# Kernel tuning notes

Measured on AMD Instinct MI355X. Metric: run time of the kernel, lower is better.

The kernel has to match this reference:

```python
import jax, jax.numpy as jnp
import numpy as np

B, T, DH, EH = 512, 64, 512, 512  # batch, window, decoder_hidden, encoder_hidden


def setup_inputs() -> dict:
    key = jax.random.key(0)
    ks = jax.random.split(key, 16)
    s = lambda *sh: 1.0 / np.sqrt(sh[-1])
    inp = {
        "X_encoded": jax.random.normal(ks[0], (B, T - 1, EH), dtype=jnp.float32),
        "y_prev": jax.random.normal(ks[1], (B, T - 1), dtype=jnp.float32),
        # attn_layer: Linear(2*DH+EH -> EH), Tanh, Linear(EH -> 1)
        "attn_W1": jax.random.normal(ks[2], (EH, 2 * DH + EH), dtype=jnp.float32) * s(2 * DH + EH),
        "attn_b1": jnp.zeros((EH,), jnp.float32),
        "attn_W2": jax.random.normal(ks[3], (1, EH), dtype=jnp.float32) * s(EH),
        "attn_b2": jnp.zeros((1,), jnp.float32),
        # fc: Linear(EH+1 -> 1), weights init normal_() in original
        "fc_W": jax.random.normal(ks[4], (1, EH + 1), dtype=jnp.float32),
        "fc_b": jnp.zeros((1,), jnp.float32),
        # LSTM(input_size=1, hidden=DH): gate order i,f,g,o
        "W_ih": jax.random.normal(ks[5], (4 * DH, 1), dtype=jnp.float32) * s(DH),
        "W_hh": jax.random.normal(ks[6], (4 * DH, DH), dtype=jnp.float32) * s(DH),
        "b_ih": jnp.zeros((4 * DH,), jnp.float32),
        "b_hh": jnp.zeros((4 * DH,), jnp.float32),
        # final heads: Linear(DH+EH -> 1) x3
        "beta_W": jax.random.normal(ks[7], (1, DH + EH), dtype=jnp.float32) * s(DH + EH),
        "beta_b": jnp.zeros((1,), jnp.float32),
        "gamma_W": jax.random.normal(ks[8], (1, DH + EH), dtype=jnp.float32) * s(DH + EH),
        "gamma_b": jnp.zeros((1,), jnp.float32),
        "sigma_W": jax.random.normal(ks[9], (1, DH + EH), dtype=jnp.float32) * s(DH + EH),
        "sigma_b": jnp.zeros((1,), jnp.float32),
    }
    return inp


def reference(X_encoded, y_prev, attn_W1, attn_b1, attn_W2, attn_b2, fc_W, fc_b,
              W_ih, W_hh, b_ih, b_hh, beta_W, beta_b, gamma_W, gamma_b, sigma_W, sigma_b):
    Bn, Tm1, eh = X_encoded.shape
    dh = W_hh.shape[1]

    def step(carry, y_t):
        d, c = carry  # [B, DH] each
        dc = jnp.concatenate([d, c], axis=-1)                      # [B, 2DH]
        x = jnp.concatenate(
            [jnp.broadcast_to(dc[:, None, :], (Bn, Tm1, 2 * dh)), X_encoded], axis=-1
        )                                                           # [B, T-1, 2DH+EH]
        h = jnp.tanh(jnp.einsum('bte,fe->btf', x, attn_W1) + attn_b1)
        scores = (jnp.einsum('btf,of->bto', h, attn_W2) + attn_b2)[..., 0]  # [B, T-1]
        beta = jax.nn.softmax(scores, axis=1)
        ctx = jnp.einsum('bt,bte->be', beta, X_encoded)             # [B, EH]
        y_tilde = jnp.concatenate([ctx, y_t[:, None]], axis=1) @ fc_W.T + fc_b  # [B, 1]
        gates = y_tilde @ W_ih.T + b_ih + d @ W_hh.T + b_hh        # [B, 4DH]
        i, f, g, o = jnp.split(gates, 4, axis=-1)
        c_new = jax.nn.sigmoid(f) * c + jax.nn.sigmoid(i) * jnp.tanh(g)
        d_new = jax.nn.sigmoid(o) * jnp.tanh(c_new)
        return (d_new, c_new), ctx

    init = (jnp.zeros((Bn, dh), X_encoded.dtype), jnp.zeros((Bn, dh), X_encoded.dtype))
    (d, c), ctxs = jax.lax.scan(step, init, y_prev.T)  # scan over T-1 steps
    ctx_last = ctxs[-1]                                # context from final iteration (pre-update d,c)
    final = jnp.concatenate([d, ctx_last], axis=1)     # [B, DH+EH]
    y_beta = final @ beta_W.T + beta_b
    y_gamma = final @ gamma_W.T + gamma_b
    y_sigma = final @ sigma_W.T + sigma_b
    return (y_beta, y_sigma, y_gamma)
```

## Files before the change

kernel.cpp:

```cpp
#include <hip/hip_runtime.h>

typedef __bf16 bf16x8 __attribute__((ext_vector_type(8)));
typedef float  f32x4  __attribute__((ext_vector_type(4)));

#define Bn  512
#define TM1 63

__device__ __forceinline__ float fast_rcp(float x){ return __builtin_amdgcn_rcpf(x); }
__device__ __forceinline__ float fast_tanh(float x){
    float e = __expf(2.0f*x);
    return 1.0f - 2.0f*fast_rcp(e + 1.0f);
}
__device__ __forceinline__ float fast_sigmoid(float x){
    return fast_rcp(1.0f + __expf(-x));
}

__device__ __forceinline__ void gll16(const __bf16* g, __bf16* l) {
    __builtin_amdgcn_global_load_lds(
        (const __attribute__((address_space(1))) unsigned int*)(g),
        (__attribute__((address_space(3))) unsigned int*)(l),
        16, 0, 0);
}


__global__ __launch_bounds__(256) void k_prep_weights(
    const float* __restrict__ W1, const float* __restrict__ Whh_f,
    const float* __restrict__ b_ih, const float* __restrict__ b_hh,
    __bf16* __restrict__ Wdc, __bf16* __restrict__ W1x, __bf16* __restrict__ Whh,
    float* __restrict__ bsum)
{
    int i = blockIdx.x*256 + threadIdx.x;
    int n = gridDim.x*256;
    for (int idx = i; idx < 512*1024; idx += n) {
        int f = idx >> 10, k = idx & 1023;
        Wdc[idx] = (__bf16)W1[f*1536 + k];
    }
    for (int idx = i; idx < 512*512; idx += n) {
        int f = idx >> 9, k = idx & 511;
        W1x[idx] = (__bf16)W1[f*1536 + 1024 + k];
    }
    for (int idx = i; idx < 2048*512; idx += n) {
        Whh[idx] = (__bf16)Whh_f[idx];
    }
    for (int idx = i; idx < 2048; idx += n) {
        bsum[idx] = b_ih[idx] + b_hh[idx];
    }
}

__global__ __launch_bounds__(256) void k_conv_x(const float* __restrict__ X, __bf16* __restrict__ Xb, int n)
{
    int idx = (blockIdx.x*256 + threadIdx.x)*4;
    if (idx < n) {
        float4 v = *(const float4*)(X + idx);
        Xb[idx+0] = (__bf16)v.x; Xb[idx+1] = (__bf16)v.y;
        Xb[idx+2] = (__bf16)v.z; Xb[idx+3] = (__bf16)v.w;
    }
}

__global__ __launch_bounds__(256) void k_xf(
    const __bf16* __restrict__ Xbf, const float* __restrict__ fcW, float* __restrict__ XF)
{
    int lane = threadIdx.x & 63, wave = threadIdx.x >> 6;
    float fcr[8];
    {
        const float4* fp = (const float4*)(fcW + lane*8);
        float4 f0 = fp[0], f1 = fp[1];
        fcr[0]=f0.x; fcr[1]=f0.y; fcr[2]=f0.z; fcr[3]=f0.w;
        fcr[4]=f1.x; fcr[5]=f1.y; fcr[6]=f1.z; fcr[7]=f1.w;
    }
    int row0 = (blockIdx.x*4 + wave)*8;
    #pragma unroll
    for (int j = 0; j < 8; ++j) {
        int row = row0 + j;
        if (row >= Bn*TM1) break;
        bf16x8 x = *(const bf16x8*)(Xbf + (size_t)row*512 + lane*8);
        float p = 0.f;
        #pragma unroll
        for (int i=0;i<8;i++) p += fcr[i]*(float)x[i];
        #pragma unroll
        for (int o=32;o;o>>=1) p += __shfl_xor(p,o,64);
        if (lane==0) XF[row] = p;
    }
}

template <int ADDBIAS>
__device__ __forceinline__ void gemm_tile_lds(
    const __bf16* __restrict__ A, const __bf16* __restrict__ Bm,
    const float* __restrict__ bias, void* __restrict__ C, int as_bf16,
    int row0, int col0, int K, int lda, int ldb, int ldc,
    __bf16* sA, __bf16* sB)
{
    int lane = threadIdx.x & 63, wave = threadIdx.x >> 6;
    int wr = wave >> 1, wc = wave & 1;
    int l15 = lane & 15, l4 = lane >> 4;
    int lr = lane >> 3;
    int lcs = ((lane & 7) ^ lr) * 8;

    auto stage = [&](int buf, int kt) {
        int k0 = kt*64;
        #pragma unroll
        for (int j = 0; j < 2; ++j) {
            int c = wave*2 + j;
            int grow = c*8 + lr;
            gll16(A  + (size_t)(row0+grow)*lda + k0 + lcs, sA + buf*4096 + c*512);
            gll16(Bm + (size_t)(col0+grow)*ldb + k0 + lcs, sB + buf*4096 + c*512);
        }
    };

    int NT = K >> 6;
    stage(0, 0);
    f32x4 acc[2][2] = {};
    int s7 = l15 & 7;
    const __bf16* aRow = sA + (wr*32 + l15)*64;
    const __bf16* bRow = sB + (wc*32 + l15)*64;
    for (int kt = 0; kt < NT; ++kt) {
        int buf = kt & 1;
        asm volatile("s_waitcnt vmcnt(0)");
        __syncthreads();
        if (kt + 1 < NT) stage(buf ^ 1, kt + 1);
        #pragma unroll
        for (int kk = 0; kk < 2; ++kk) {
            int ch = ((l4 + kk*4) ^ s7) * 8;
            bf16x8 a0 = *(const bf16x8*)(aRow + buf*4096 + ch);
            bf16x8 a1 = *(const bf16x8*)(aRow + buf*4096 + 16*64 + ch);
            bf16x8 b0 = *(const bf16x8*)(bRow + buf*4096 + ch);
            bf16x8 b1 = *(const bf16x8*)(bRow + buf*4096 + 16*64 + ch);
            acc[0][0] = __builtin_amdgcn_mfma_f32_16x16x32_bf16(a0,b0,acc[0][0],0,0,0);
            acc[0][1] = __builtin_amdgcn_mfma_f32_16x16x32_bf16(a0,b1,acc[0][1],0,0,0);
            acc[1][0] = __builtin_amdgcn_mfma_f32_16x16x32_bf16(a1,b0,acc[1][0],0,0,0);
            acc[1][1] = __builtin_amdgcn_mfma_f32_16x16x32_bf16(a1,b1,acc[1][1],0,0,0);
        }
    }
    int row_a = row0 + wr*32;
    int col_b = col0 + wc*32;
    #pragma unroll
    for (int mi=0; mi<2; mi++)
    #pragma unroll
    for (int ni=0; ni<2; ni++) {
        int r0 = row_a + mi*16 + l4*4;
        int c0 = col_b + ni*16 + l15;
        float bv = ADDBIAS ? bias[c0] : 0.f;
        if (as_bf16) {
            __bf16* Cb = (__bf16*)C;
            #pragma unroll
            for (int r=0; r<4; r++)
                Cb[(size_t)(r0+r)*ldc + c0] = (__bf16)(acc[mi][ni][r] + bv);
        } else {
            float* Cf = (float*)C;
            #pragma unroll
            for (int r=0; r<4; r++)
                Cf[(size_t)(r0+r)*ldc + c0] = acc[mi][ni][r];
        }
    }
}

__global__ __launch_bounds__(256) void k_gemm_xw(
    const __bf16* __restrict__ A, const __bf16* __restrict__ Bm,
    const float* __restrict__ bias, __bf16* __restrict__ C)
{
    __shared__ __bf16 sA[2*4096], sB[2*4096];
    int orig = (blockIdx.x & 7)*504 + (blockIdx.x >> 3);
    int tm = orig >> 3, tn = orig & 7;
    gemm_tile_lds<1>(A, Bm, bias, C, 1, tm*64, tn*64, 512, 512, 512, 512, sA, sB);
}

__global__ __launch_bounds__(256) void k_step_gemm(
    const __bf16* __restrict__ dc, const __bf16* __restrict__ Wdc,
    const __bf16* __restrict__ Whh, __bf16* __restrict__ dcWp, __bf16* __restrict__ dWhhp)
{
    __shared__ __bf16 sA[2*4096], sB[2*4096];
    int blk = blockIdx.x;
    if (blk < 256) {
        int kh = blk & 3, tt = blk >> 2;
        int tm = tt >> 3, tn = tt & 7;
        gemm_tile_lds<0>(dc + kh*256, Wdc + kh*256, nullptr,
                         dcWp + (size_t)kh*512*512, 1,
                         tm*64, tn*64, 256, 1024, 1024, 512, sA, sB);
    } else {
        int b2 = blk - 256;
        int kh = b2 & 1, tt = b2 >> 1;
        int tm = tt >> 5, tn = tt & 31;
        gemm_tile_lds<0>(dc + kh*256, Whh + kh*256, nullptr,
                         dWhhp + (size_t)kh*512*2048, 1,
                         tm*64, tn*64, 256, 1024, 512, 2048, sA, sB);
    }
}


#define PSTR 76
__global__ __launch_bounds__(512) void k_step_fused(
    int t,
    const __bf16* __restrict__ dcWp, const __bf16* __restrict__ dWhhp,
    const __bf16* __restrict__ XWb, const float* __restrict__ XF,
    const float* __restrict__ y_prev, const float* __restrict__ W2,
    const float* __restrict__ fcW, const float* __restrict__ fcb,
    const float* __restrict__ W_ih, const float* __restrict__ bsum,
    float* __restrict__ c_f32, float* __restrict__ d_f32,
    __bf16* __restrict__ dc_bf16, float* __restrict__ beta_out)
{
    int b = blockIdx.x;
    int tid = threadIdx.x, lane = tid & 63, wave = tid >> 6;
    __shared__ float s_part[64*PSTR];
    __shared__ float s_sc[64];
    __shared__ float s_y;

    size_t gb = (size_t)b*2048 + tid;
    const __bf16* dW0 = dWhhp;
    const __bf16* dW1 = dWhhp + (size_t)512*2048;
    float pg_i = (float)dW0[gb]        + (float)dW1[gb];
    float pg_f = (float)dW0[gb + 512]  + (float)dW1[gb + 512];
    float pg_g = (float)dW0[gb + 1024] + (float)dW1[gb + 1024];
    float pg_o = (float)dW0[gb + 1536] + (float)dW1[gb + 1536];
    float wi_i = W_ih[tid];
    float wi_f = W_ih[512 + tid];
    float wi_g = W_ih[1024 + tid];
    float wi_o = W_ih[1536 + tid];
    float bs_i = bsum[tid];
    float bs_f = bsum[512 + tid];
    float bs_g = bsum[1024 + tid];
    float bs_o = bsum[1536 + tid];
    float c_old = c_f32[(size_t)b*512 + tid];

    float w2r[8], dr[8];
    {
        const float4* w2p = (const float4*)(W2 + lane*8);
        float4 w0 = w2p[0], w1 = w2p[1];
        w2r[0]=w0.x; w2r[1]=w0.y; w2r[2]=w0.z; w2r[3]=w0.w;
        w2r[4]=w1.x; w2r[5]=w1.y; w2r[6]=w1.z; w2r[7]=w1.w;
        #pragma unroll
        for (int i=0;i<8;i++) dr[i] = 0.f;
        #pragma unroll
        for (int q=0;q<4;q++) {
            bf16x8 a = *(const bf16x8*)(dcWp + (size_t)q*512*512 + (size_t)b*512 + lane*8);
            #pragma unroll
            for (int i=0;i<8;i++) dr[i] += (float)a[i];
        }
    }
    {
        const __bf16* xwp = XWb + ((size_t)b*TM1 + wave*8)*512 + lane*8;
        #pragma unroll
        for (int j = 0; j < 8; ++j) {
            int tt = wave*8 + j;
            float p = 0.f;
            if (tt < TM1) {
                bf16x8 xw = *(const bf16x8*)(xwp + (size_t)j*512);
                #pragma unroll
                for (int i=0;i<8;i++) p += w2r[i]*fast_tanh(dr[i] + (float)xw[i]);
            }
            s_part[tt*PSTR + lane] = p;
        }
    }
    __syncthreads();
    {
        int tt = tid >> 3, g = tid & 7;
        const float4* pp = (const float4*)(s_part + tt*PSTR + g*8);
        float4 u0 = pp[0], u1 = pp[1];
        float r = u0.x+u0.y+u0.z+u0.w + u1.x+u1.y+u1.z+u1.w;
        r += __shfl_xor(r, 1, 64);
        r += __shfl_xor(r, 2, 64);
        r += __shfl_xor(r, 4, 64);
        if (g == 0) s_sc[tt] = r;
    }
    __syncthreads();
    if (wave == 0) {
        float e = (lane < TM1) ? __expf(s_sc[lane]) : 0.f;
        float sum = e;
        #pragma unroll
        for (int o=32;o;o>>=1) sum += __shfl_xor(sum,o,64);
        float beta = e*fast_rcp(sum);
        if (t == 62) beta_out[b*64 + lane] = beta;
        float yp = (lane < TM1) ? beta*XF[(size_t)b*TM1 + lane] : 0.f;
        #pragma unroll
        for (int o=32;o;o>>=1) yp += __shfl_xor(yp,o,64);
        if (lane == 0)
            s_y = yp + fcW[512]*y_prev[(size_t)b*TM1 + t] + fcb[0];
    }
    __syncthreads();
    float yv = s_y;
    {
        int k = tid;
        float gi = pg_i + yv*wi_i + bs_i;
        float gf = pg_f + yv*wi_f + bs_f;
        float gg = pg_g + yv*wi_g + bs_g;
        float go = pg_o + yv*wi_o + bs_o;
        size_t sk = (size_t)b*512 + k;
        float cn = fast_sigmoid(gf)*c_old + fast_sigmoid(gi)*fast_tanh(gg);
        float dn = fast_sigmoid(go)*fast_tanh(cn);
        c_f32[sk] = cn; d_f32[sk] = dn;
        dc_bf16[(size_t)b*1024 + k]       = (__bf16)dn;
        dc_bf16[(size_t)b*1024 + 512 + k] = (__bf16)cn;
    }
}

__global__ __launch_bounds__(512) void k_finish(
    const float* __restrict__ beta62, const __bf16* __restrict__ Xbf,
    const float* __restrict__ d_f32,
    const float* __restrict__ bW, const float* __restrict__ bb,
    const float* __restrict__ sW, const float* __restrict__ sb,
    const float* __restrict__ gW, const float* __restrict__ gb,
    float* __restrict__ out)
{
    int b = blockIdx.x;
    int tid = threadIdx.x, lane = tid & 63, wave = tid >> 6;
    __shared__ float s_beta[64];
    __shared__ float s_red[3][8];
    if (tid < 64) s_beta[tid] = beta62[b*64 + tid];
    __syncthreads();
    float ctxv = 0.f;
    {
        const __bf16* xp = Xbf + (size_t)b*TM1*512 + tid;
        #pragma unroll
        for (int tt = 0; tt < TM1; ++tt)
            ctxv += s_beta[tt]*(float)xp[(size_t)tt*512];
    }
    float dv = d_f32[(size_t)b*512 + tid];
    float pb = bW[tid]*dv + bW[512+tid]*ctxv;
    float ps = sW[tid]*dv + sW[512+tid]*ctxv;
    float pg = gW[tid]*dv + gW[512+tid]*ctxv;
    #pragma unroll
    for (int o=32;o;o>>=1) {
        pb += __shfl_xor(pb,o,64); ps += __shfl_xor(ps,o,64); pg += __shfl_xor(pg,o,64);
    }
    if (lane==0) { s_red[0][wave]=pb; s_red[1][wave]=ps; s_red[2][wave]=pg; }
    __syncthreads();
    if (tid==0) {
        float sb_=0,ss_=0,sg_=0;
        #pragma unroll
        for (int w=0;w<8;w++){ sb_+=s_red[0][w]; ss_+=s_red[1][w]; sg_+=s_red[2][w]; }
        out[b]        = sb_ + bb[0];
        out[512 + b]  = ss_ + sb[0];
        out[1024 + b] = sg_ + gb[0];
    }
}

extern "C" void kernel_launch(void* const* d_in, const int* in_sizes, int n_in,
                              void* d_out, int out_size, void* d_ws, size_t ws_size,
                              hipStream_t stream) {
    const float* X      = (const float*)d_in[0];
    const float* y_prev = (const float*)d_in[1];
    const float* W1     = (const float*)d_in[2];
    const float* b1     = (const float*)d_in[3];
    const float* W2     = (const float*)d_in[4];
    const float* fcW    = (const float*)d_in[6];
    const float* fcb    = (const float*)d_in[7];
    const float* W_ih   = (const float*)d_in[8];
    const float* W_hh_f = (const float*)d_in[9];
    const float* b_ih   = (const float*)d_in[10];
    const float* b_hh   = (const float*)d_in[11];
    const float* betaW  = (const float*)d_in[12];
    const float* betab  = (const float*)d_in[13];
    const float* gammaW = (const float*)d_in[14];
    const float* gammab = (const float*)d_in[15];
    const float* sigmaW = (const float*)d_in[16];
    const float* sigmab = (const float*)d_in[17];
    float* out = (float*)d_out;

    size_t off = 0;
    char* ws = (char*)d_ws;
    auto alloc = [&](size_t bytes) { void* p = ws + off; off += (bytes + 255) & ~(size_t)255; return p; };
    __bf16* XWb  = (__bf16*)alloc((size_t)Bn*TM1*512*2);
    __bf16* Xbf  = (__bf16*)alloc((size_t)Bn*TM1*512*2);
    __bf16* Wdc  = (__bf16*)alloc((size_t)512*1024*2);
    __bf16* W1x  = (__bf16*)alloc((size_t)512*512*2);
    __bf16* Whh  = (__bf16*)alloc((size_t)2048*512*2);
    __bf16* dcb  = (__bf16*)alloc((size_t)Bn*1024*2);
    float*  cf   = (float*)alloc((size_t)Bn*512*4);
    float*  df   = (float*)alloc((size_t)Bn*512*4);
    __bf16* dcWp = (__bf16*)alloc((size_t)4*512*512*2);
    __bf16* dWhhp= (__bf16*)alloc((size_t)2*512*2048*2);
    float*  bsum = (float*)alloc((size_t)2048*4);
    float*  XF   = (float*)alloc((size_t)Bn*TM1*4);
    float*  b62  = (float*)alloc((size_t)Bn*64*4);

    hipMemsetAsync(dcb, 0, (size_t)Bn*1024*2, stream);
    hipMemsetAsync(cf,  0, (size_t)Bn*512*4, stream);

    k_prep_weights<<<512, 256, 0, stream>>>(W1, W_hh_f, b_ih, b_hh, Wdc, W1x, Whh, bsum);
    int nx = Bn*TM1*512;
    k_conv_x<<<(nx/4 + 255)/256, 256, 0, stream>>>(X, Xbf, nx);
    k_xf<<<(Bn*TM1 + 31)/32, 256, 0, stream>>>(Xbf, fcW, XF);
    k_gemm_xw<<<(Bn*TM1/64)*8, 256, 0, stream>>>(Xbf, W1x, b1, XWb);

    for (int t = 0; t < TM1; ++t) {
        k_step_gemm<<<768, 256, 0, stream>>>(dcb, Wdc, Whh, dcWp, dWhhp);
        k_step_fused<<<Bn, 512, 0, stream>>>(t, dcWp, dWhhp, XWb, XF, y_prev, W2,
                                             fcW, fcb, W_ih, bsum,
                                             cf, df, dcb, b62);
    }
    k_finish<<<Bn, 512, 0, stream>>>(b62, Xbf, df,
                                     betaW, betab, sigmaW, sigmab, gammaW, gammab, out);
}
```

Measured before the change: 1.169 ms.

## Fuse X bf16 conversion with fc dot and enlarge XW GEMM tile to 128 rows

Merges the fp32-to-bf16 conversion of X_encoded with the per-row fc dot product into one kernel. The fc dot is now computed from the fp32 values, which avoids a second pass over the bf16 copy. The precomputed X·W1x GEMM is rewritten with a dedicated 128x64 tile, so each wave computes 2x4 MFMA blocks. That raises reuse of the B tile and halves the block count, at the cost of more LDS per block. These setup kernels run once, and the 63-step loop that dominates the runtime is untouched.

```diff
diff --git a/kernel.cpp b/kernel.cpp
--- a/kernel.cpp
+++ b/kernel.cpp
@@ -47,18 +47,9 @@
     }
 }
 
-__global__ __launch_bounds__(256) void k_conv_x(const float* __restrict__ X, __bf16* __restrict__ Xb, int n)
-{
-    int idx = (blockIdx.x*256 + threadIdx.x)*4;
-    if (idx < n) {
-        float4 v = *(const float4*)(X + idx);
-        Xb[idx+0] = (__bf16)v.x; Xb[idx+1] = (__bf16)v.y;
-        Xb[idx+2] = (__bf16)v.z; Xb[idx+3] = (__bf16)v.w;
-    }
-}
-
-__global__ __launch_bounds__(256) void k_xf(
-    const __bf16* __restrict__ Xbf, const float* __restrict__ fcW, float* __restrict__ XF)
+__global__ __launch_bounds__(256) void k_conv_xf(
+    const float* __restrict__ X, const float* __restrict__ fcW,
+    __bf16* __restrict__ Xb, float* __restrict__ XF)
 {
     int lane = threadIdx.x & 63, wave = threadIdx.x >> 6;
     float fcr[8];
@@ -68,19 +59,19 @@
         fcr[0]=f0.x; fcr[1]=f0.y; fcr[2]=f0.z; fcr[3]=f0.w;
         fcr[4]=f1.x; fcr[5]=f1.y; fcr[6]=f1.z; fcr[7]=f1.w;
     }
-    int row0 = (blockIdx.x*4 + wave)*8;
-    #pragma unroll
-    for (int j = 0; j < 8; ++j) {
-        int row = row0 + j;
-        if (row >= Bn*TM1) break;
-        bf16x8 x = *(const bf16x8*)(Xbf + (size_t)row*512 + lane*8);
-        float p = 0.f;
-        #pragma unroll
-        for (int i=0;i<8;i++) p += fcr[i]*(float)x[i];
-        #pragma unroll
-        for (int o=32;o;o>>=1) p += __shfl_xor(p,o,64);
-        if (lane==0) XF[row] = p;
-    }
+    int row = blockIdx.x*4 + wave;
+    if (row >= Bn*TM1) return;
+    const float4* xp = (const float4*)(X + (size_t)row*512 + lane*8);
+    float4 v0 = xp[0], v1 = xp[1];
+    bf16x8 xb;
+    xb[0]=(__bf16)v0.x; xb[1]=(__bf16)v0.y; xb[2]=(__bf16)v0.z; xb[3]=(__bf16)v0.w;
+    xb[4]=(__bf16)v1.x; xb[5]=(__bf16)v1.y; xb[6]=(__bf16)v1.z; xb[7]=(__bf16)v1.w;
+    *(bf16x8*)(Xb + (size_t)row*512 + lane*8) = xb;
+    float p = fcr[0]*v0.x + fcr[1]*v0.y + fcr[2]*v0.z + fcr[3]*v0.w
+            + fcr[4]*v1.x + fcr[5]*v1.y + fcr[6]*v1.z + fcr[7]*v1.w;
+    #pragma unroll
+    for (int o=32;o;o>>=1) p += __shfl_xor(p,o,64);
+    if (lane==0) XF[row] = p;
 }
 
 template <int ADDBIAS>
@@ -158,10 +149,72 @@
     const __bf16* __restrict__ A, const __bf16* __restrict__ Bm,
     const float* __restrict__ bias, __bf16* __restrict__ C)
 {
-    __shared__ __bf16 sA[2*4096], sB[2*4096];
-    int orig = (blockIdx.x & 7)*504 + (blockIdx.x >> 3);
+    __shared__ __bf16 sA[2*8192];
+    __shared__ __bf16 sB[2*4096];
+    int orig = (blockIdx.x & 7)*252 + (blockIdx.x >> 3);
     int tm = orig >> 3, tn = orig & 7;
-    gemm_tile_lds<1>(A, Bm, bias, C, 1, tm*64, tn*64, 512, 512, 512, 512, sA, sB);
+    int row0 = tm*128, col0 = tn*64;
+    int lane = threadIdx.x & 63, wave = threadIdx.x >> 6;
+    int l15 = lane & 15, l4 = lane >> 4;
+    int lr = lane >> 3;
+    int lcs = ((lane & 7) ^ lr) * 8;
+
+    auto stage = [&](int buf, int kt) {
+        int k0 = kt*64;
+        #pragma unroll
+        for (int j = 0; j < 4; ++j) {
+            int c = wave*4 + j;
+            int grow = c*8 + lr;
+            gll16(A + (size_t)(row0+grow)*512 + k0 + lcs, sA + buf*8192 + c*512);
+        }
+        #pragma unroll
+        for (int j = 0; j < 2; ++j) {
+            int c = wave*2 + j;
+            int grow = c*8 + lr;
+            gll16(Bm + (size_t)(col0+grow)*512 + k0 + lcs, sB + buf*4096 + c*512);
+        }
+    };
+
+    stage(0, 0);
+    f32x4 acc[2][4] = {};
+    int s7 = l15 & 7;
+    const __bf16* aRow = sA + (wave*32 + l15)*64;
+    const __bf16* bRow = sB + l15*64;
+    for (int kt = 0; kt < 8; ++kt) {
+        int buf = kt & 1;
+        asm volatile("s_waitcnt vmcnt(0)");
+        __syncthreads();
+        if (kt + 1 < 8) stage(buf ^ 1, kt + 1);
+        #pragma unroll
+        for (int kk = 0; kk < 2; ++kk) {
+            int ch = ((l4 + kk*4) ^ s7) * 8;
+            bf16x8 a0 = *(const bf16x8*)(aRow + buf*8192 + ch);
+            bf16x8 a1 = *(const bf16x8*)(aRow + buf*8192 + 16*64 + ch);
+            bf16x8 b0 = *(const bf16x8*)(bRow + buf*4096 + ch);
+            bf16x8 b1 = *(const bf16x8*)(bRow + buf*4096 + 16*64 + ch);
+            bf16x8 b2 = *(const bf16x8*)(bRow + buf*4096 + 32*64 + ch);
+            bf16x8 b3 = *(const bf16x8*)(bRow + buf*4096 + 48*64 + ch);
+            acc[0][0] = __builtin_amdgcn_mfma_f32_16x16x32_bf16(a0,b0,acc[0][0],0,0,0);
+            acc[0][1] = __builtin_amdgcn_mfma_f32_16x16x32_bf16(a0,b1,acc[0][1],0,0,0);
+            acc[0][2] = __builtin_amdgcn_mfma_f32_16x16x32_bf16(a0,b2,acc[0][2],0,0,0);
+            acc[0][3] = __builtin_amdgcn_mfma_f32_16x16x32_bf16(a0,b3,acc[0][3],0,0,0);
+            acc[1][0] = __builtin_amdgcn_mfma_f32_16x16x32_bf16(a1,b0,acc[1][0],0,0,0);
+            acc[1][1] = __builtin_amdgcn_mfma_f32_16x16x32_bf16(a1,b1,acc[1][1],0,0,0);
+            acc[1][2] = __builtin_amdgcn_mfma_f32_16x16x32_bf16(a1,b2,acc[1][2],0,0,0);
+            acc[1][3] = __builtin_amdgcn_mfma_f32_16x16x32_bf16(a1,b3,acc[1][3],0,0,0);
+        }
+    }
+    #pragma unroll
+    for (int mi=0; mi<2; mi++)
+    #pragma unroll
+    for (int ni=0; ni<4; ni++) {
+        int r0 = row0 + wave*32 + mi*16 + l4*4;
+        int c0 = col0 + ni*16 + l15;
+        float bv = bias[c0];
+        #pragma unroll
+        for (int r=0; r<4; r++)
+            C[(size_t)(r0+r)*512 + c0] = (__bf16)(acc[mi][ni][r] + bv);
+    }
 }
 
 __global__ __launch_bounds__(256) void k_step_gemm(
@@ -376,10 +429,8 @@
     hipMemsetAsync(cf,  0, (size_t)Bn*512*4, stream);
 
     k_prep_weights<<<512, 256, 0, stream>>>(W1, W_hh_f, b_ih, b_hh, Wdc, W1x, Whh, bsum);
-    int nx = Bn*TM1*512;
-    k_conv_x<<<(nx/4 + 255)/256, 256, 0, stream>>>(X, Xbf, nx);
-    k_xf<<<(Bn*TM1 + 31)/32, 256, 0, stream>>>(Xbf, fcW, XF);
-    k_gemm_xw<<<(Bn*TM1/64)*8, 256, 0, stream>>>(Xbf, W1x, b1, XWb);
+    k_conv_xf<<<(Bn*TM1 + 3)/4, 256, 0, stream>>>(X, fcW, Xbf, XF);
+    k_gemm_xw<<<(Bn*TM1/128)*8, 256, 0, stream>>>(Xbf, W1x, b1, XWb);
 
     for (int t = 0; t < TM1; ++t) {
         k_step_gemm<<<768, 256, 0, stream>>>(dcb, Wdc, Whh, dcWp, dWhhp);
```

Measured after the change: 1.162 ms. Within noise of the previous version (-0.6%).
